# Kernel tuning notes

Hardware: AMD Instinct MI355X
Metric: run time of the kernel (lower is better)

The kernel has to match this reference:

```python
import jax, jax.numpy as jnp
import numpy as np

WIN_H, WIN_W = 8, 8
NUM_HEADS = 32


def _relative_position_index(wh: int, ww: int) -> np.ndarray:
    # Swin V1 style pairwise relative position index, [wh*ww, wh*ww]
    coords = np.stack(np.meshgrid(np.arange(wh), np.arange(ww), indexing='ij'))  # [2, wh, ww]
    cf = coords.reshape(2, -1)                      # [2, N]
    rel = cf[:, :, None] - cf[:, None, :]           # [2, N, N]
    rel = rel.transpose(1, 2, 0).copy()             # [N, N, 2]
    rel[:, :, 0] += wh - 1
    rel[:, :, 1] += ww - 1
    rel[:, :, 0] *= 2 * ww - 1
    return rel.sum(-1)                              # [N, N]


def setup_inputs() -> dict:
    key = jax.random.key(0)
    ks = jax.random.split(key, 6)
    B, N, C = 2048, WIN_H * WIN_W, 256
    return {
        'x': jax.random.normal(ks[0], (B, N, C), dtype=jnp.float32),
        'w_qkv': jax.random.normal(ks[1], (3 * C, C), dtype=jnp.float32) * 0.02,
        'b_qkv': jax.random.normal(ks[2], (3 * C,), dtype=jnp.float32) * 0.02,
        'w_proj': jax.random.normal(ks[3], (C, C), dtype=jnp.float32) * 0.02,
        'b_proj': jax.random.normal(ks[4], (C,), dtype=jnp.float32) * 0.02,
        'bias_table': jax.random.normal(ks[5], ((2 * WIN_H - 1) * (2 * WIN_W - 1), NUM_HEADS), dtype=jnp.float32) * 0.02,
    }


def reference(x, w_qkv, b_qkv, w_proj, b_proj, bias_table):
    B, N, C = x.shape
    H = NUM_HEADS
    d = C // H
    idx = jnp.asarray(_relative_position_index(WIN_H, WIN_W).reshape(-1))  # [N*N] int
    # gathered relative positional bias: [H, N, N]
    bias = bias_table[idx].reshape(N, N, H).transpose(2, 0, 1)
    # qkv projection -> [3, B, H, N, d]
    qkv = (x @ w_qkv.T + b_qkv).reshape(B, N, 3, H, d).transpose(2, 0, 3, 1, 4)
    q, k, v = qkv[0], qkv[1], qkv[2]
    # NOTE: torch code normalizes over dim=1 == HEAD axis (faithful quirk),
    # and self.scale is never applied in forward.
    def norm_heads(t):
        n = jnp.sqrt(jnp.sum(t * t, axis=1, keepdims=True))
        return t / jnp.maximum(n, 1e-12)
    q = norm_heads(q)
    k = norm_heads(k)
    logits = jnp.einsum('bhqd,bhkd->bhqk', q, k) + bias[None]  # [B,H,N,N]
    attn = jax.nn.softmax(logits, axis=-1)
    out = jnp.einsum('bhqk,bhkd->bhqd', attn, v)               # [B,H,N,d]
    out = out.transpose(0, 2, 1, 3).reshape(B, N, C)
    return out @ w_proj.T + b_proj
```

## Files before the change

### kernel.cpp

```cpp
#include <hip/hip_runtime.h>

typedef __attribute__((ext_vector_type(4))) float f32x4;
typedef __attribute__((ext_vector_type(8))) short s16x8;
typedef __attribute__((ext_vector_type(4))) short s16x4;

#define NWIN 2048

__device__ __forceinline__ ushort f2bf(float f) {
    union { float f; unsigned u; } v; v.f = f;
    unsigned r = v.u + 0x7FFFu + ((v.u >> 16) & 1u);
    return (ushort)(r >> 16);
}
__device__ __forceinline__ float bf2f(ushort u) {
    union { unsigned u; float f; } v; v.u = ((unsigned)u) << 16;
    return v.f;
}
__device__ __forceinline__ unsigned pk2(float a, float b) {
    return (unsigned)f2bf(a) | ((unsigned)f2bf(b) << 16);
}
union BF4 { unsigned u[2]; s16x4 v; };

__global__ void prep_kernel(const float* __restrict__ wqkv,
                            const float* __restrict__ wproj,
                            const float* __restrict__ btab,
                            ushort* __restrict__ wq,
                            ushort* __restrict__ wp,
                            ushort* __restrict__ bb) {
    int t = blockIdx.x * 256 + threadIdx.x;
    if (t < 196608) {
        wq[t] = f2bf(wqkv[t]);
    } else if (t < 262144) {
        int i = t - 196608;
        wp[i] = f2bf(wproj[i]);
    } else if (t < 393216) {
        int i = t - 262144;
        int h  = i >> 12;
        int rem = i & 4095;
        int qi = rem >> 6;
        int kj = rem & 63;
        int rh = (qi >> 3) - (kj >> 3) + 7;
        int rw = (qi & 7)  - (kj & 7)  + 7;
        bb[i] = f2bf(btab[(rh * 15 + rw) * 32 + h]);
    }
}

__global__ __launch_bounds__(512, 4) void attn_kernel(
    const float* __restrict__ x,
    const float* __restrict__ bqkv,
    const float* __restrict__ bproj,
    const ushort* __restrict__ wq,
    const ushort* __restrict__ wp,
    const ushort* __restrict__ biasb,
    float* __restrict__ out)
{
    __shared__ ushort sX[64 * 256];
    __shared__ float  sN[1024];

    const int tid  = threadIdx.x;
    const int lane = tid & 63;
    const int w    = tid >> 6;
    const int g    = lane >> 4;
    const int c    = lane & 15;
    const int b    = blockIdx.x;

    const f32x4 fz = {0.f, 0.f, 0.f, 0.f};
    const s16x4 z4 = {0, 0, 0, 0};

    sN[tid] = 0.f; sN[tid + 512] = 0.f;

    {
        const float4* xg = (const float4*)(x + (size_t)b * 16384);
        #pragma unroll
        for (int it = 0; it < 8; ++it) {
            int i = tid + it * 512;
            float4 v = xg[i];
            int row = i >> 6;
            int col = (i & 63) << 2;
            int bo = (row * 512 + col * 2) ^ ((row & 7) << 4);
            ushort4 u;
            u.x = f2bf(v.x); u.y = f2bf(v.y); u.z = f2bf(v.z); u.w = f2bf(v.w);
            *(ushort4*)((char*)sX + bo) = u;
        }
    }
    __syncthreads();

    s16x4 vpk[4][2];
    {
        f32x4 acc[4][2];
        #pragma unroll
        for (int mi = 0; mi < 4; ++mi) { acc[mi][0] = fz; acc[mi][1] = fz; }
        #pragma unroll
        for (int ks = 0; ks < 8; ++ks) {
            s16x8 af[4];
            #pragma unroll
            for (int mi = 0; mi < 4; ++mi) {
                int row = 16 * mi + c;
                int bo = (row * 512 + ks * 64 + g * 16) ^ ((row & 7) << 4);
                af[mi] = *(const s16x8*)((const char*)sX + bo);
            }
            s16x8 wv[2];
            #pragma unroll
            for (int nj = 0; nj < 2; ++nj)
                wv[nj] = *(const s16x8*)(wq + (512 + 32 * w + 16 * nj + c) * 256 + ks * 32 + g * 8);
            #pragma unroll
            for (int mi = 0; mi < 4; ++mi)
                #pragma unroll
                for (int nj = 0; nj < 2; ++nj)
                    acc[mi][nj] = __builtin_amdgcn_mfma_f32_16x16x32_bf16(af[mi], wv[nj], acc[mi][nj], 0, 0, 0);
        }
        #pragma unroll
        for (int nj = 0; nj < 2; ++nj) {
            float bv = bqkv[512 + 32 * w + 16 * nj + c];
            #pragma unroll
            for (int mi = 0; mi < 4; ++mi) {
                BF4 t;
                t.u[0] = pk2(acc[mi][nj][0] + bv, acc[mi][nj][1] + bv);
                t.u[1] = pk2(acc[mi][nj][2] + bv, acc[mi][nj][3] + bv);
                vpk[mi][nj] = t.v;
            }
        }
    }

    s16x4 kpk[2][4];
    {
        f32x4 ac[2][4];
        #pragma unroll
        for (int mt = 0; mt < 2; ++mt)
            #pragma unroll
            for (int nt = 0; nt < 4; ++nt) ac[mt][nt] = fz;
        #pragma unroll
        for (int ks = 0; ks < 8; ++ks) {
            s16x8 af[4];
            #pragma unroll
            for (int nt = 0; nt < 4; ++nt) {
                int row = 16 * nt + c;
                int bo = (row * 512 + ks * 64 + g * 16) ^ ((row & 7) << 4);
                af[nt] = *(const s16x8*)((const char*)sX + bo);
            }
            s16x8 wk[2];
            #pragma unroll
            for (int mt = 0; mt < 2; ++mt)
                wk[mt] = *(const s16x8*)(wq + (256 + 32 * w + 16 * mt + c) * 256 + ks * 32 + g * 8);
            #pragma unroll
            for (int mt = 0; mt < 2; ++mt)
                #pragma unroll
                for (int nt = 0; nt < 4; ++nt)
                    ac[mt][nt] = __builtin_amdgcn_mfma_f32_16x16x32_bf16(wk[mt], af[nt], ac[mt][nt], 0, 0, 0);
        }
        f32x4 bk0 = *(const f32x4*)(bqkv + 256 + 32 * w + 4 * g);
        f32x4 bk1 = *(const f32x4*)(bqkv + 256 + 32 * w + 16 + 4 * g);
        #pragma unroll
        for (int nt = 0; nt < 4; ++nt) { ac[0][nt] += bk0; ac[1][nt] += bk1; }
        #pragma unroll
        for (int nt = 0; nt < 4; ++nt) {
            #pragma unroll
            for (int j = 0; j < 4; ++j) {
                float p = ac[0][nt][j] * ac[0][nt][j] + ac[1][nt][j] * ac[1][nt][j];
                p += __shfl_xor(p, 32);
                if (g < 2) atomicAdd(&sN[(16 * nt + c) * 8 + 4 * g + j + 512], p);
            }
            #pragma unroll
            for (int mt = 0; mt < 2; ++mt) {
                BF4 t;
                t.u[0] = pk2(ac[mt][nt][0], ac[mt][nt][1]);
                t.u[1] = pk2(ac[mt][nt][2], ac[mt][nt][3]);
                kpk[mt][nt] = t.v;
            }
        }
    }

    s16x4 qpk[2][4];
    {
        f32x4 ac[2][4];
        #pragma unroll
        for (int mt = 0; mt < 2; ++mt)
            #pragma unroll
            for (int nt = 0; nt < 4; ++nt) ac[mt][nt] = fz;
        #pragma unroll
        for (int ks = 0; ks < 8; ++ks) {
            s16x8 af[4];
            #pragma unroll
            for (int nt = 0; nt < 4; ++nt) {
                int row = 16 * nt + c;
                int bo = (row * 512 + ks * 64 + g * 16) ^ ((row & 7) << 4);
                af[nt] = *(const s16x8*)((const char*)sX + bo);
            }
            s16x8 wqa[2];
            #pragma unroll
            for (int mt = 0; mt < 2; ++mt)
                wqa[mt] = *(const s16x8*)(wq + (32 * w + 16 * mt + c) * 256 + ks * 32 + g * 8);
            #pragma unroll
            for (int mt = 0; mt < 2; ++mt)
                #pragma unroll
                for (int nt = 0; nt < 4; ++nt)
                    ac[mt][nt] = __builtin_amdgcn_mfma_f32_16x16x32_bf16(wqa[mt], af[nt], ac[mt][nt], 0, 0, 0);
        }
        f32x4 bq0 = *(const f32x4*)(bqkv + 32 * w + 4 * g);
        f32x4 bq1 = *(const f32x4*)(bqkv + 32 * w + 16 + 4 * g);
        #pragma unroll
        for (int nt = 0; nt < 4; ++nt) { ac[0][nt] += bq0; ac[1][nt] += bq1; }
        #pragma unroll
        for (int nt = 0; nt < 4; ++nt) {
            #pragma unroll
            for (int j = 0; j < 4; ++j) {
                float p = ac[0][nt][j] * ac[0][nt][j] + ac[1][nt][j] * ac[1][nt][j];
                p += __shfl_xor(p, 32);
                if (g < 2) atomicAdd(&sN[(16 * nt + c) * 8 + 4 * g + j], p);
            }
            #pragma unroll
            for (int mt = 0; mt < 2; ++mt) {
                BF4 t;
                t.u[0] = pk2(ac[mt][nt][0], ac[mt][nt][1]);
                t.u[1] = pk2(ac[mt][nt][2], ac[mt][nt][3]);
                qpk[mt][nt] = t.v;
            }
        }
    }
    __syncthreads();

    #pragma unroll
    for (int nt = 0; nt < 4; ++nt) {
        float iq[4], ik[4];
        #pragma unroll
        for (int j = 0; j < 4; ++j) {
            int a = (16 * nt + c) * 8 + ((4 * g + j) & 7);
            iq[j] = 1.f / fmaxf(sqrtf(sN[a]), 1e-12f);
            ik[j] = 1.f / fmaxf(sqrtf(sN[a + 512]), 1e-12f);
        }
        #pragma unroll
        for (int mt = 0; mt < 2; ++mt) {
            BF4 t; t.v = qpk[mt][nt];
            t.u[0] = pk2(bf2f((ushort)(t.u[0] & 0xffff)) * iq[0],
                         bf2f((ushort)(t.u[0] >> 16))    * iq[1]);
            t.u[1] = pk2(bf2f((ushort)(t.u[1] & 0xffff)) * iq[2],
                         bf2f((ushort)(t.u[1] >> 16))    * iq[3]);
            qpk[mt][nt] = t.v;
            t.v = kpk[mt][nt];
            t.u[0] = pk2(bf2f((ushort)(t.u[0] & 0xffff)) * ik[0],
                         bf2f((ushort)(t.u[0] >> 16))    * ik[1]);
            t.u[1] = pk2(bf2f((ushort)(t.u[1] & 0xffff)) * ik[2],
                         bf2f((ushort)(t.u[1] >> 16))    * ik[3]);
            kpk[mt][nt] = t.v;
        }
    }

    #pragma unroll
    for (int hi = 0; hi < 4; ++hi) {
        const int mt = hi >> 1, par = hi & 1, h = 4 * w + hi;
        const bool keepq = par ? (g >= 2) : (g < 2);
        s16x4 vf[4];
        #pragma unroll
        for (int kv = 0; kv < 4; ++kv) {
            BF4 t; t.v = vpk[kv][mt];
            if (par) {
                t.u[0] = (unsigned)__shfl_xor((int)t.u[0], 8);
                t.u[1] = (unsigned)__shfl_xor((int)t.u[1], 8);
            }
            vf[kv] = (c < 8) ? t.v : z4;
        }
        const ushort* bh = biasb + h * 4096;
        #pragma unroll
        for (int tqh = 0; tqh < 2; ++tqh) {
            f32x4 S[4][2];
            #pragma unroll
            for (int t2 = 0; t2 < 2; ++t2) {
                s16x4 qf = keepq ? qpk[mt][2 * tqh + t2] : z4;
                #pragma unroll
                for (int tk = 0; tk < 4; ++tk)
                    S[tk][t2] = __builtin_amdgcn_mfma_f32_16x16x16bf16_1k(kpk[mt][tk], qf, fz, 0, 0, 0);
            }
            float rinv[2];
            #pragma unroll
            for (int t2 = 0; t2 < 2; ++t2) {
                float sum = 0.f;
                #pragma unroll
                for (int tk = 0; tk < 4; ++tk) {
                    ushort4 bv4 = *(const ushort4*)(bh + (16 * (2 * tqh + t2) + c) * 64 + 16 * tk + 4 * g);
                    float e0 = __expf(S[tk][t2][0] + bf2f(bv4.x));
                    float e1 = __expf(S[tk][t2][1] + bf2f(bv4.y));
                    float e2 = __expf(S[tk][t2][2] + bf2f(bv4.z));
                    float e3 = __expf(S[tk][t2][3] + bf2f(bv4.w));
                    S[tk][t2][0] = e0; S[tk][t2][1] = e1;
                    S[tk][t2][2] = e2; S[tk][t2][3] = e3;
                    sum += e0 + e1 + e2 + e3;
                }
                sum += __shfl_xor(sum, 16);
                sum += __shfl_xor(sum, 32);
                rinv[t2] = 1.f / sum;
            }
            #pragma unroll
            for (int t2 = 0; t2 < 2; ++t2) {
                f32x4 o = fz;
                #pragma unroll
                for (int kv = 0; kv < 4; ++kv) {
                    BF4 pa;
                    pa.u[0] = pk2(S[kv][t2][0] * rinv[t2], S[kv][t2][1] * rinv[t2]);
                    pa.u[1] = pk2(S[kv][t2][2] * rinv[t2], S[kv][t2][3] * rinv[t2]);
                    o = __builtin_amdgcn_mfma_f32_16x16x16bf16_1k(pa.v, vf[kv], o, 0, 0, 0);
                }
                if (c < 8) {
                    #pragma unroll
                    for (int j = 0; j < 4; ++j) {
                        int tok = 16 * (2 * tqh + t2) + 4 * g + j;
                        int bo = (tok * 512 + (h * 8 + c) * 2) ^ ((tok & 7) << 4);
                        *(ushort*)((char*)sX + bo) = f2bf(o[j]);
                    }
                }
            }
        }
    }
    __syncthreads();

    {
        f32x4 pacc[4][2];
        #pragma unroll
        for (int mi = 0; mi < 4; ++mi) { pacc[mi][0] = fz; pacc[mi][1] = fz; }
        #pragma unroll
        for (int ks = 0; ks < 8; ++ks) {
            s16x8 af[4];
            #pragma unroll
            for (int mi = 0; mi < 4; ++mi) {
                int row = 16 * mi + c;
                int bo = (row * 512 + ks * 64 + g * 16) ^ ((row & 7) << 4);
                af[mi] = *(const s16x8*)((const char*)sX + bo);
            }
            s16x8 wfr[2];
            #pragma unroll
            for (int nj = 0; nj < 2; ++nj)
                wfr[nj] = *(const s16x8*)(wp + (32 * w + 16 * nj + c) * 256 + ks * 32 + g * 8);
            #pragma unroll
            for (int mi = 0; mi < 4; ++mi)
                #pragma unroll
                for (int nj = 0; nj < 2; ++nj)
                    pacc[mi][nj] = __builtin_amdgcn_mfma_f32_16x16x32_bf16(af[mi], wfr[nj], pacc[mi][nj], 0, 0, 0);
        }
        float* og = out + (size_t)b * 16384;
        #pragma unroll
        for (int nj = 0; nj < 2; ++nj) {
            int col = 32 * w + 16 * nj + c;
            float bp = bproj[col];
            #pragma unroll
            for (int mi = 0; mi < 4; ++mi)
                #pragma unroll
                for (int j = 0; j < 4; ++j)
                    og[(16 * mi + 4 * g + j) * 256 + col] = pacc[mi][nj][j] + bp;
        }
    }
}

extern "C" void kernel_launch(void* const* d_in, const int* in_sizes, int n_in,
                              void* d_out, int out_size, void* d_ws, size_t ws_size,
                              hipStream_t stream) {
    const float* x     = (const float*)d_in[0];
    const float* wqkv  = (const float*)d_in[1];
    const float* bqkv  = (const float*)d_in[2];
    const float* wproj = (const float*)d_in[3];
    const float* bproj = (const float*)d_in[4];
    const float* btab  = (const float*)d_in[5];

    ushort* wq_b   = (ushort*)d_ws;
    ushort* wp_b   = wq_b + 196608;
    ushort* bias_b = wp_b + 65536;

    prep_kernel<<<1536, 256, 0, stream>>>(wqkv, wproj, btab, wq_b, wp_b, bias_b);
    attn_kernel<<<NWIN, 512, 0, stream>>>(x, bqkv, bproj, wq_b, wp_b, bias_b,
                                          (float*)d_out);
}
```

Measured before the change: 445.1 us.

## Stage V in shared memory and process one query tile at a time

V projection results are no longer held in registers and shuffled between lanes. They are written to a new swizzled shared buffer and read back per head. The attention loop now handles one 16-row query tile per iteration instead of two, which lowers the number of live score registers. Launch bounds drop from 4 to 3 blocks per CU to match the larger shared-memory footprint. The trade is extra LDS traffic and fewer resident blocks in exchange for lower register pressure and no cross-lane shuffles.

```diff
diff --git a/kernel.cpp b/kernel.cpp
--- a/kernel.cpp
+++ b/kernel.cpp
@@ -18,7 +18,7 @@
 __device__ __forceinline__ unsigned pk2(float a, float b) {
     return (unsigned)f2bf(a) | ((unsigned)f2bf(b) << 16);
 }
-union BF4 { unsigned u[2]; s16x4 v; };
+union BF4 { unsigned u[2]; unsigned long long ull; s16x4 v; };
 
 __global__ void prep_kernel(const float* __restrict__ wqkv,
                             const float* __restrict__ wproj,
@@ -44,7 +44,7 @@
     }
 }
 
-__global__ __launch_bounds__(512, 4) void attn_kernel(
+__global__ __launch_bounds__(512, 3) void attn_kernel(
     const float* __restrict__ x,
     const float* __restrict__ bqkv,
     const float* __restrict__ bproj,
@@ -54,6 +54,7 @@
     float* __restrict__ out)
 {
     __shared__ ushort sX[64 * 256];
+    __shared__ ushort sV[32 * 8 * 64];
     __shared__ float  sN[1024];
 
     const int tid  = threadIdx.x;
@@ -84,7 +85,6 @@
     }
     __syncthreads();
 
-    s16x4 vpk[4][2];
     {
         f32x4 acc[4][2];
         #pragma unroll
@@ -110,13 +110,16 @@
         }
         #pragma unroll
         for (int nj = 0; nj < 2; ++nj) {
-            float bv = bqkv[512 + 32 * w + 16 * nj + c];
+            int vc = 32 * w + 16 * nj + c;
+            float bv = bqkv[512 + vc];
+            int hh = vc >> 3, dd = vc & 7;
             #pragma unroll
             for (int mi = 0; mi < 4; ++mi) {
                 BF4 t;
                 t.u[0] = pk2(acc[mi][nj][0] + bv, acc[mi][nj][1] + bv);
                 t.u[1] = pk2(acc[mi][nj][2] + bv, acc[mi][nj][3] + bv);
-                vpk[mi][nj] = t.v;
+                int bo = (hh * 1024 + dd * 128 + 32 * mi + 8 * g) ^ (dd << 4);
+                *(unsigned long long*)((char*)sV + bo) = t.ull;
             }
         }
     }
@@ -251,60 +254,48 @@
         s16x4 vf[4];
         #pragma unroll
         for (int kv = 0; kv < 4; ++kv) {
-            BF4 t; t.v = vpk[kv][mt];
-            if (par) {
-                t.u[0] = (unsigned)__shfl_xor((int)t.u[0], 8);
-                t.u[1] = (unsigned)__shfl_xor((int)t.u[1], 8);
-            }
-            vf[kv] = (c < 8) ? t.v : z4;
+            if (c < 8) {
+                int bo = (h * 1024 + c * 128 + 32 * kv + 8 * g) ^ (c << 4);
+                BF4 t; t.ull = *(const unsigned long long*)((const char*)sV + bo);
+                vf[kv] = t.v;
+            } else vf[kv] = z4;
         }
         const ushort* bh = biasb + h * 4096;
         #pragma unroll
-        for (int tqh = 0; tqh < 2; ++tqh) {
-            f32x4 S[4][2];
-            #pragma unroll
-            for (int t2 = 0; t2 < 2; ++t2) {
-                s16x4 qf = keepq ? qpk[mt][2 * tqh + t2] : z4;
-                #pragma unroll
-                for (int tk = 0; tk < 4; ++tk)
-                    S[tk][t2] = __builtin_amdgcn_mfma_f32_16x16x16bf16_1k(kpk[mt][tk], qf, fz, 0, 0, 0);
-            }
-            float rinv[2];
-            #pragma unroll
-            for (int t2 = 0; t2 < 2; ++t2) {
-                float sum = 0.f;
-                #pragma unroll
-                for (int tk = 0; tk < 4; ++tk) {
-                    ushort4 bv4 = *(const ushort4*)(bh + (16 * (2 * tqh + t2) + c) * 64 + 16 * tk + 4 * g);
-                    float e0 = __expf(S[tk][t2][0] + bf2f(bv4.x));
-                    float e1 = __expf(S[tk][t2][1] + bf2f(bv4.y));
-                    float e2 = __expf(S[tk][t2][2] + bf2f(bv4.z));
-                    float e3 = __expf(S[tk][t2][3] + bf2f(bv4.w));
-                    S[tk][t2][0] = e0; S[tk][t2][1] = e1;
-                    S[tk][t2][2] = e2; S[tk][t2][3] = e3;
-                    sum += e0 + e1 + e2 + e3;
-                }
-                sum += __shfl_xor(sum, 16);
-                sum += __shfl_xor(sum, 32);
-                rinv[t2] = 1.f / sum;
-            }
-            #pragma unroll
-            for (int t2 = 0; t2 < 2; ++t2) {
-                f32x4 o = fz;
-                #pragma unroll
-                for (int kv = 0; kv < 4; ++kv) {
-                    BF4 pa;
-                    pa.u[0] = pk2(S[kv][t2][0] * rinv[t2], S[kv][t2][1] * rinv[t2]);
-                    pa.u[1] = pk2(S[kv][t2][2] * rinv[t2], S[kv][t2][3] * rinv[t2]);
-                    o = __builtin_amdgcn_mfma_f32_16x16x16bf16_1k(pa.v, vf[kv], o, 0, 0, 0);
-                }
-                if (c < 8) {
-                    #pragma unroll
-                    for (int j = 0; j < 4; ++j) {
-                        int tok = 16 * (2 * tqh + t2) + 4 * g + j;
-                        int bo = (tok * 512 + (h * 8 + c) * 2) ^ ((tok & 7) << 4);
-                        *(ushort*)((char*)sX + bo) = f2bf(o[j]);
-                    }
+        for (int tq = 0; tq < 4; ++tq) {
+            s16x4 qf = keepq ? qpk[mt][tq] : z4;
+            f32x4 S[4];
+            #pragma unroll
+            for (int tk = 0; tk < 4; ++tk)
+                S[tk] = __builtin_amdgcn_mfma_f32_16x16x16bf16_1k(kpk[mt][tk], qf, fz, 0, 0, 0);
+            float sum = 0.f;
+            #pragma unroll
+            for (int tk = 0; tk < 4; ++tk) {
+                ushort4 bv4 = *(const ushort4*)(bh + (16 * tq + c) * 64 + 16 * tk + 4 * g);
+                float e0 = __expf(S[tk][0] + bf2f(bv4.x));
+                float e1 = __expf(S[tk][1] + bf2f(bv4.y));
+                float e2 = __expf(S[tk][2] + bf2f(bv4.z));
+                float e3 = __expf(S[tk][3] + bf2f(bv4.w));
+                S[tk][0] = e0; S[tk][1] = e1; S[tk][2] = e2; S[tk][3] = e3;
+                sum += e0 + e1 + e2 + e3;
+            }
+            sum += __shfl_xor(sum, 16);
+            sum += __shfl_xor(sum, 32);
+            float rinv = 1.f / sum;
+            f32x4 o = fz;
+            #pragma unroll
+            for (int kv = 0; kv < 4; ++kv) {
+                BF4 pa;
+                pa.u[0] = pk2(S[kv][0] * rinv, S[kv][1] * rinv);
+                pa.u[1] = pk2(S[kv][2] * rinv, S[kv][3] * rinv);
+                o = __builtin_amdgcn_mfma_f32_16x16x16bf16_1k(pa.v, vf[kv], o, 0, 0, 0);
+            }
+            if (c < 8) {
+                #pragma unroll
+                for (int j = 0; j < 4; ++j) {
+                    int tok = 16 * tq + 4 * g + j;
+                    int bo = (tok * 512 + (h * 8 + c) * 2) ^ ((tok & 7) << 4);
+                    *(ushort*)((char*)sX + bo) = f2bf(o[j]);
                 }
             }
         }
```

After: 444.7 us. No clear change (-0.1%).
